# Kernel optimization log

Measured on AMD Instinct MI355X. Metric: run time of the kernel, lower is better.

## Reference

```python
import jax, jax.numpy as jnp
import numpy as np

# Static CT geometry (ctlib-style): parallel-beam pixel-driven backprojection
VIEWS, DETS = 512, 512   # sinogram: angles x detector bins
H, W = 256, 256          # reconstructed image grid


def setup_inputs() -> dict:
    key = jax.random.key(0)
    proj = jax.random.normal(key, (4, 1, VIEWS, DETS), dtype=jnp.float32)
    # options = [dImg (pixel size), dDet (detector bin size), Ang0, dAng]
    options = jnp.array([1.0, 1.5, 0.0, np.pi / VIEWS], dtype=jnp.float32)
    return {"proj": proj, "options": options}


def reference(proj, options):
    # proj: [B, 1, VIEWS, DETS] sinogram; returns image [B, 1, H, W]
    dImg, dDet, ang0, dAng = options[0], options[1], options[2], options[3]

    ang = ang0 + dAng * jnp.arange(VIEWS, dtype=jnp.float32)          # [V]
    cos_a, sin_a = jnp.cos(ang), jnp.sin(ang)
    # pixel-center world coordinates (y axis points up)
    xs = (jnp.arange(W, dtype=jnp.float32) - (W - 1) / 2.0) * dImg     # [W]
    ys = ((H - 1) / 2.0 - jnp.arange(H, dtype=jnp.float32)) * dImg     # [H]

    # signed distance of each pixel to the detector axis for each view: t[v,y,x]
    t = cos_a[:, None, None] * xs[None, None, :] + sin_a[:, None, None] * ys[None, :, None]
    u = t / dDet + (DETS - 1) / 2.0                                    # fractional detector coord

    i0 = jnp.floor(u)
    w = u - i0                                                         # linear interp weight
    i0i = i0.astype(jnp.int32)
    i1i = i0i + 1
    m0 = ((i0i >= 0) & (i0i < DETS)).astype(proj.dtype)
    m1 = ((i1i >= 0) & (i1i < DETS)).astype(proj.dtype)
    i0c = jnp.clip(i0i, 0, DETS - 1)
    i1c = jnp.clip(i1i, 0, DETS - 1)

    p = proj[:, 0]                                                     # [B, V, D]
    vix = jnp.arange(VIEWS)[:, None, None]                             # [V,1,1]
    p0 = p[:, vix, i0c]                                                # [B, V, H, W]
    p1 = p[:, vix, i1c]
    val = p0 * ((1.0 - w) * m0) + p1 * (w * m1)                        # interpolated ray values

    img = dAng * jnp.sum(val, axis=1)                                  # accumulate over views
    return img[:, None, :, :]
```

## Files before the change

kernel.cpp:

```cpp
#include <hip/hip_runtime.h>
#include <hip/hip_bf16.h>
#include <math.h>

#define VIEWS  512
#define DETS   512
#define HH     256
#define WW     256
#define VSPLIT 16
#define VCHUNK (VIEWS / VSPLIT)
#define TS     32
#define WIN    48

typedef float v2f __attribute__((ext_vector_type(2)));

__global__ __launch_bounds__(256, 4) void backproj_kernel(
    const float* __restrict__ proj,
    const float* __restrict__ options,
    float* __restrict__ out)
{
    __shared__ float2 s_cs[VCHUNK];
    __shared__ float4 s_pk[VCHUNK];
    __shared__ uint2  s_w2[VCHUNK][WIN];

    const float dImg = options[0];
    const float dDet = options[1];
    const float ang0 = options[2];
    const float dAng = options[3];

    const int tid  = threadIdx.x;
    const int blk  = blockIdx.x;
    const int vq   = blk & 15;
    const int tile = blk >> 4;
    const int v0   = vq * VCHUNK;
    const int x0t  = (tile & 7) * TS;
    const int y0t  = (tile >> 3) * TS;

    if (tid < VCHUNK) {
        float s, c;
        sincosf(ang0 + dAng * (float)(v0 + tid), &s, &c);
        s_cs[tid] = make_float2(c, s);
    }
    __syncthreads();

    const float sc   = dImg / dDet;
    const float uoff = (DETS - 1) * 0.5f;

    const float xa = ((float)x0t - (WW - 1) * 0.5f) * sc;
    const float xb = ((float)(x0t + TS - 1) - (WW - 1) * 0.5f) * sc;
    const float ya = (HH - 1) * 0.5f - (float)y0t;
    const float yb = (HH - 1) * 0.5f - (float)(y0t + TS - 1);

#pragma unroll
    for (int r = 0; r < 3; ++r) {
        int item = tid + 256 * r;
        int view = item / 24;
        int slot = item - view * 24;
        float2 cs = s_cs[view];
        float c  = cs.x;
        float dd = cs.y * sc;
        float umin = fminf(c * xa, c * xb) + fminf(dd * ya, dd * yb) + uoff;
        int w0a = (((int)floorf(umin)) - 2) & ~3;
        if (slot == 0)
            s_pk[view] = make_float4(c, dd, uoff - (float)w0a,
                                     3.0f * fmaxf(dd, 0.0f));
        const float* p0r = proj + (size_t)(v0 + view) * DETS + w0a + 2 * slot;
        float2 qa = *(const float2*)(p0r);
        float2 qb = *(const float2*)(p0r + 1 * VIEWS * DETS);
        float2 qc = *(const float2*)(p0r + 2 * VIEWS * DETS);
        float2 qd = *(const float2*)(p0r + 3 * VIEWS * DETS);
        __hip_bfloat162 h01a = __float22bfloat162_rn(make_float2(qa.x, qb.x));
        __hip_bfloat162 h23a = __float22bfloat162_rn(make_float2(qc.x, qd.x));
        __hip_bfloat162 h01b = __float22bfloat162_rn(make_float2(qa.y, qb.y));
        __hip_bfloat162 h23b = __float22bfloat162_rn(make_float2(qc.y, qd.y));
        uint4 dw;
        dw.x = (uint32_t)__bfloat16_as_ushort(h01a.x)
             | ((uint32_t)__bfloat16_as_ushort(h01a.y) << 16);
        dw.y = (uint32_t)__bfloat16_as_ushort(h23a.x)
             | ((uint32_t)__bfloat16_as_ushort(h23a.y) << 16);
        dw.z = (uint32_t)__bfloat16_as_ushort(h01b.x)
             | ((uint32_t)__bfloat16_as_ushort(h01b.y) << 16);
        dw.w = (uint32_t)__bfloat16_as_ushort(h23b.x)
             | ((uint32_t)__bfloat16_as_ushort(h23b.y) << 16);
        *(uint4*)&s_w2[view][2 * slot] = dw;
    }

    const int xl = tid & 31;
    const int yg = tid >> 5;
    const float xsc  = ((float)(x0t + xl) - (WW - 1) * 0.5f) * sc;
    const float ys0u = (HH - 1) * 0.5f - (float)(y0t + yg * 4);

    __syncthreads();

    const v2f zero = 0.0f;
    const v2f onev = 1.0f;
    v2f a0A = 0.f, a0B = 0.f, a1A = 0.f, a1B = 0.f;
    v2f a2A = 0.f, a2B = 0.f, a3A = 0.f, a3B = 0.f;
    float aq0 = 0.f, aq1 = 0.f, aq2 = 0.f, aq3 = 0.f;

#pragma unroll 4
    for (int vv = 0; vv < VCHUNK; ++vv) {
        float4 pk = s_pk[vv];
        float dd = pk.y;
        float tb = fmaf(pk.x, xsc, pk.z);
        float u0 = fmaf(dd, ys0u, tb);
        float mF = floorf(u0 - pk.w);
        int   mi = (int)mF;
        float f0 = u0 - mF;
        v2f fA; fA.x = f0;        fA.y = f0 - dd;
        v2f fB = fA - 2.0f * dd;
        v2f wA0 = __builtin_elementwise_min(__builtin_elementwise_max(fA, zero), onev);
        v2f wA1 = __builtin_elementwise_min(__builtin_elementwise_max(fA - 1.0f, zero), onev);
        v2f wA2 = __builtin_elementwise_min(__builtin_elementwise_max(fA - 2.0f, zero), onev);
        v2f wB0 = __builtin_elementwise_min(__builtin_elementwise_max(fB, zero), onev);
        v2f wB1 = __builtin_elementwise_min(__builtin_elementwise_max(fB - 1.0f, zero), onev);
        v2f wB2 = __builtin_elementwise_min(__builtin_elementwise_max(fB - 2.0f, zero), onev);
        const uint2* wp = &s_w2[vv][mi];
        uint2 t0 = wp[0];
        uint2 t1 = wp[1];
        uint2 t2 = wp[2];
        uint2 t3 = wp[3];
        uint32_t p0 = t0.x, p1 = t1.x, p2 = t2.x, p3 = t3.x;
        uint32_t r0 = t0.y, r1 = t1.y, r2 = t2.y, r3 = t3.y;
        {
            float q0 = __uint_as_float(p0 << 16), q1 = __uint_as_float(p1 << 16);
            float q2 = __uint_as_float(p2 << 16), q3 = __uint_as_float(p3 << 16);
            float d0 = q1 - q0, d1 = q2 - q1, d2 = q3 - q2;
            aq0 += q0;
            a0A = __builtin_elementwise_fma(wA0, (v2f)d0,
                  __builtin_elementwise_fma(wA1, (v2f)d1,
                  __builtin_elementwise_fma(wA2, (v2f)d2, a0A)));
            a0B = __builtin_elementwise_fma(wB0, (v2f)d0,
                  __builtin_elementwise_fma(wB1, (v2f)d1,
                  __builtin_elementwise_fma(wB2, (v2f)d2, a0B)));
        }
        {
            float q0 = __uint_as_float(p0 & 0xFFFF0000u), q1 = __uint_as_float(p1 & 0xFFFF0000u);
            float q2 = __uint_as_float(p2 & 0xFFFF0000u), q3 = __uint_as_float(p3 & 0xFFFF0000u);
            float d0 = q1 - q0, d1 = q2 - q1, d2 = q3 - q2;
            aq1 += q0;
            a1A = __builtin_elementwise_fma(wA0, (v2f)d0,
                  __builtin_elementwise_fma(wA1, (v2f)d1,
                  __builtin_elementwise_fma(wA2, (v2f)d2, a1A)));
            a1B = __builtin_elementwise_fma(wB0, (v2f)d0,
                  __builtin_elementwise_fma(wB1, (v2f)d1,
                  __builtin_elementwise_fma(wB2, (v2f)d2, a1B)));
        }
        {
            float q0 = __uint_as_float(r0 << 16), q1 = __uint_as_float(r1 << 16);
            float q2 = __uint_as_float(r2 << 16), q3 = __uint_as_float(r3 << 16);
            float d0 = q1 - q0, d1 = q2 - q1, d2 = q3 - q2;
            aq2 += q0;
            a2A = __builtin_elementwise_fma(wA0, (v2f)d0,
                  __builtin_elementwise_fma(wA1, (v2f)d1,
                  __builtin_elementwise_fma(wA2, (v2f)d2, a2A)));
            a2B = __builtin_elementwise_fma(wB0, (v2f)d0,
                  __builtin_elementwise_fma(wB1, (v2f)d1,
                  __builtin_elementwise_fma(wB2, (v2f)d2, a2B)));
        }
        {
            float q0 = __uint_as_float(r0 & 0xFFFF0000u), q1 = __uint_as_float(r1 & 0xFFFF0000u);
            float q2 = __uint_as_float(r2 & 0xFFFF0000u), q3 = __uint_as_float(r3 & 0xFFFF0000u);
            float d0 = q1 - q0, d1 = q2 - q1, d2 = q3 - q2;
            aq3 += q0;
            a3A = __builtin_elementwise_fma(wA0, (v2f)d0,
                  __builtin_elementwise_fma(wA1, (v2f)d1,
                  __builtin_elementwise_fma(wA2, (v2f)d2, a3A)));
            a3B = __builtin_elementwise_fma(wB0, (v2f)d0,
                  __builtin_elementwise_fma(wB1, (v2f)d1,
                  __builtin_elementwise_fma(wB2, (v2f)d2, a3B)));
        }
    }

    const size_t prow = (size_t)(y0t + yg * 4) * WW + x0t + xl;
    float* o0 = out + 0 * (HH * WW) + prow;
    float* o1 = out + 1 * (HH * WW) + prow;
    float* o2 = out + 2 * (HH * WW) + prow;
    float* o3 = out + 3 * (HH * WW) + prow;
    atomicAdd(o0,          (a0A.x + aq0) * dAng);
    atomicAdd(o0 + WW,     (a0A.y + aq0) * dAng);
    atomicAdd(o0 + 2 * WW, (a0B.x + aq0) * dAng);
    atomicAdd(o0 + 3 * WW, (a0B.y + aq0) * dAng);
    atomicAdd(o1,          (a1A.x + aq1) * dAng);
    atomicAdd(o1 + WW,     (a1A.y + aq1) * dAng);
    atomicAdd(o1 + 2 * WW, (a1B.x + aq1) * dAng);
    atomicAdd(o1 + 3 * WW, (a1B.y + aq1) * dAng);
    atomicAdd(o2,          (a2A.x + aq2) * dAng);
    atomicAdd(o2 + WW,     (a2A.y + aq2) * dAng);
    atomicAdd(o2 + 2 * WW, (a2B.x + aq2) * dAng);
    atomicAdd(o2 + 3 * WW, (a2B.y + aq2) * dAng);
    atomicAdd(o3,          (a3A.x + aq3) * dAng);
    atomicAdd(o3 + WW,     (a3A.y + aq3) * dAng);
    atomicAdd(o3 + 2 * WW, (a3B.x + aq3) * dAng);
    atomicAdd(o3 + 3 * WW, (a3B.y + aq3) * dAng);
}

extern "C" void kernel_launch(void* const* d_in, const int* in_sizes, int n_in,
                              void* d_out, int out_size, void* d_ws, size_t ws_size,
                              hipStream_t stream) {
    const float* proj    = (const float*)d_in[0];
    const float* options = (const float*)d_in[1];
    float* out = (float*)d_out;

    hipMemsetAsync(d_out, 0, (size_t)out_size * sizeof(float), stream);

    dim3 grid(64 * VSPLIT);
    dim3 block(256);
    backproj_kernel<<<grid, block, 0, stream>>>(proj, options, out);
}
```

Baseline: 79.17 us.

## Replace atomic accumulation with per-split workspace partials and a reduction kernel

Each view-chunk block now writes its partial sums with plain stores into a separate slice of a workspace buffer, and a second kernel sums the 16 slices with float4 loads and applies the dAng scale. This drops the memset and the 16-way contended float atomics on the output. In exchange it adds a second launch and extra global traffic: about 16 MB written and read back through the workspace. It also makes the summation order deterministic.

```diff
diff --git a/kernel.cpp b/kernel.cpp
--- a/kernel.cpp
+++ b/kernel.cpp
@@ -10,13 +10,14 @@
 #define VCHUNK (VIEWS / VSPLIT)
 #define TS     32
 #define WIN    48
+#define NPIX   (4 * HH * WW)
 
 typedef float v2f __attribute__((ext_vector_type(2)));
 
 __global__ __launch_bounds__(256, 4) void backproj_kernel(
     const float* __restrict__ proj,
     const float* __restrict__ options,
-    float* __restrict__ out)
+    float* __restrict__ ws)
 {
     __shared__ float2 s_cs[VCHUNK];
     __shared__ float4 s_pk[VCHUNK];
@@ -25,7 +26,6 @@
     const float dImg = options[0];
     const float dDet = options[1];
     const float ang0 = options[2];
-    const float dAng = options[3];
 
     const int tid  = threadIdx.x;
     const int blk  = blockIdx.x;
@@ -37,7 +37,7 @@
 
     if (tid < VCHUNK) {
         float s, c;
-        sincosf(ang0 + dAng * (float)(v0 + tid), &s, &c);
+        sincosf(ang0 + options[3] * (float)(v0 + tid), &s, &c);
         s_cs[tid] = make_float2(c, s);
     }
     __syncthreads();
@@ -171,27 +171,42 @@
         }
     }
 
-    const size_t prow = (size_t)(y0t + yg * 4) * WW + x0t + xl;
-    float* o0 = out + 0 * (HH * WW) + prow;
-    float* o1 = out + 1 * (HH * WW) + prow;
-    float* o2 = out + 2 * (HH * WW) + prow;
-    float* o3 = out + 3 * (HH * WW) + prow;
-    atomicAdd(o0,          (a0A.x + aq0) * dAng);
-    atomicAdd(o0 + WW,     (a0A.y + aq0) * dAng);
-    atomicAdd(o0 + 2 * WW, (a0B.x + aq0) * dAng);
-    atomicAdd(o0 + 3 * WW, (a0B.y + aq0) * dAng);
-    atomicAdd(o1,          (a1A.x + aq1) * dAng);
-    atomicAdd(o1 + WW,     (a1A.y + aq1) * dAng);
-    atomicAdd(o1 + 2 * WW, (a1B.x + aq1) * dAng);
-    atomicAdd(o1 + 3 * WW, (a1B.y + aq1) * dAng);
-    atomicAdd(o2,          (a2A.x + aq2) * dAng);
-    atomicAdd(o2 + WW,     (a2A.y + aq2) * dAng);
-    atomicAdd(o2 + 2 * WW, (a2B.x + aq2) * dAng);
-    atomicAdd(o2 + 3 * WW, (a2B.y + aq2) * dAng);
-    atomicAdd(o3,          (a3A.x + aq3) * dAng);
-    atomicAdd(o3 + WW,     (a3A.y + aq3) * dAng);
-    atomicAdd(o3 + 2 * WW, (a3B.x + aq3) * dAng);
-    atomicAdd(o3 + 3 * WW, (a3B.y + aq3) * dAng);
+    float* o = ws + (size_t)vq * NPIX
+                  + ((size_t)(y0t + yg * 4)) * WW + x0t + xl;
+    o[0 * (size_t)(HH * WW) + 0 * WW] = a0A.x + aq0;
+    o[0 * (size_t)(HH * WW) + 1 * WW] = a0A.y + aq0;
+    o[0 * (size_t)(HH * WW) + 2 * WW] = a0B.x + aq0;
+    o[0 * (size_t)(HH * WW) + 3 * WW] = a0B.y + aq0;
+    o[1 * (size_t)(HH * WW) + 0 * WW] = a1A.x + aq1;
+    o[1 * (size_t)(HH * WW) + 1 * WW] = a1A.y + aq1;
+    o[1 * (size_t)(HH * WW) + 2 * WW] = a1B.x + aq1;
+    o[1 * (size_t)(HH * WW) + 3 * WW] = a1B.y + aq1;
+    o[2 * (size_t)(HH * WW) + 0 * WW] = a2A.x + aq2;
+    o[2 * (size_t)(HH * WW) + 1 * WW] = a2A.y + aq2;
+    o[2 * (size_t)(HH * WW) + 2 * WW] = a2B.x + aq2;
+    o[2 * (size_t)(HH * WW) + 3 * WW] = a2B.y + aq2;
+    o[3 * (size_t)(HH * WW) + 0 * WW] = a3A.x + aq3;
+    o[3 * (size_t)(HH * WW) + 1 * WW] = a3A.y + aq3;
+    o[3 * (size_t)(HH * WW) + 2 * WW] = a3B.x + aq3;
+    o[3 * (size_t)(HH * WW) + 3 * WW] = a3B.y + aq3;
+}
+
+__global__ __launch_bounds__(256) void reduce_kernel(
+    const float* __restrict__ ws,
+    const float* __restrict__ options,
+    float* __restrict__ out)
+{
+    const float dAng = options[3];
+    const int i4 = blockIdx.x * 256 + threadIdx.x;
+    const float4* w = (const float4*)ws;
+    float4 a = w[i4];
+#pragma unroll
+    for (int q = 1; q < VSPLIT; ++q) {
+        float4 p = w[(size_t)q * (NPIX / 4) + i4];
+        a.x += p.x; a.y += p.y; a.z += p.z; a.w += p.w;
+    }
+    a.x *= dAng; a.y *= dAng; a.z *= dAng; a.w *= dAng;
+    ((float4*)out)[i4] = a;
 }
 
 extern "C" void kernel_launch(void* const* d_in, const int* in_sizes, int n_in,
@@ -200,10 +215,12 @@
     const float* proj    = (const float*)d_in[0];
     const float* options = (const float*)d_in[1];
     float* out = (float*)d_out;
-
-    hipMemsetAsync(d_out, 0, (size_t)out_size * sizeof(float), stream);
+    float* ws  = (float*)d_ws;
 
     dim3 grid(64 * VSPLIT);
     dim3 block(256);
-    backproj_kernel<<<grid, block, 0, stream>>>(proj, options, out);
+    backproj_kernel<<<grid, block, 0, stream>>>(proj, options, ws);
+
+    dim3 rgrid(NPIX / 4 / 256);
+    reduce_kernel<<<rgrid, block, 0, stream>>>(ws, options, out);
 }
```

Result: slower. 86.10 us (+8.7%).
